# Optimization experiments

Hardware: AMD Instinct MI355X
Metric: run time of the kernel (lower is better)

The kernel has to match this reference:

```python
import jax, jax.numpy as jnp
import numpy as np

BIN_ALPHA = 1.0  # alpha mixture factor from init
NEG_SLOPE = 0.1  # LeakyReLU slope


def setup_inputs() -> dict:
    key = jax.random.key(0)
    ks = jax.random.split(key, 10)
    B, N, BIN, D = 8, 19264, 100, 768
    gene_expression = jax.random.uniform(ks[0], (B, N), dtype=jnp.float32) * 10.0
    pad_mask = jax.random.randint(ks[1], (B, N), 0, 2, dtype=jnp.int32)
    masked_mask = jax.random.randint(ks[2], (B, N), 0, 2, dtype=jnp.int32)
    # layer1: Linear(1, BIN) -> weight (BIN,1) stored as (BIN,), bias (BIN,)
    w1 = jax.random.normal(ks[3], (BIN,), dtype=jnp.float32) * (1.0)
    b1 = jax.random.normal(ks[4], (BIN,), dtype=jnp.float32) * 0.1
    # layer2: Linear(BIN, BIN) -> weight (BIN,BIN), bias (BIN,)
    w2 = jax.random.normal(ks[5], (BIN, BIN), dtype=jnp.float32) * (1.0 / np.sqrt(BIN))
    b2 = jax.random.normal(ks[6], (BIN,), dtype=jnp.float32) * 0.1
    emb_table = jax.random.normal(ks[7], (BIN, D), dtype=jnp.float32)
    pad_emb = jax.random.normal(ks[8], (D,), dtype=jnp.float32)
    mask_emb = jax.random.normal(ks[9], (D,), dtype=jnp.float32)
    return {
        "gene_expression": gene_expression,
        "pad_mask": pad_mask,
        "masked_mask": masked_mask,
        "w1": w1, "b1": b1, "w2": w2, "b2": b2,
        "emb_table": emb_table, "pad_emb": pad_emb, "mask_emb": mask_emb,
    }


def reference(gene_expression, pad_mask, masked_mask, w1, b1, w2, b2,
              emb_table, pad_emb, mask_emb):
    # v1 = Linear(1, BIN): x[..., None] * w1 + b1 -> (B, N, BIN)
    v1 = gene_expression[..., None] * w1 + b1
    # LeakyReLU(0.1)
    v2 = jnp.where(v1 > 0, v1, NEG_SLOPE * v1)
    # cross-layer projection: v3 = alpha * v2 + Linear(BIN, BIN)(v2)
    v3 = BIN_ALPHA * v2 + jnp.einsum("bnk,jk->bnj", v2, w2) + b2
    weights = jax.nn.softmax(v3, axis=-1)          # (B, N, BIN)
    embeddings = jnp.einsum("bnk,kd->bnd", weights, emb_table)  # (B, N, D)
    # mixed_precision=True: pad/mask token embeddings are cast to bfloat16
    # before being scattered into the float32 output (then upcast on assign).
    pad_e = pad_emb.astype(jnp.bfloat16).astype(embeddings.dtype)
    mask_e = mask_emb.astype(jnp.bfloat16).astype(embeddings.dtype)
    embeddings = jnp.where((pad_mask != 0)[..., None], pad_e, embeddings)
    embeddings = jnp.where((masked_mask != 0)[..., None], mask_e, embeddings)
    return embeddings
```

## Files before the change

### kernel.cpp

```cpp
#include <hip/hip_runtime.h>
#include <hip/hip_bf16.h>

#define BINS 100
#define DIM 768
#define TPB 64
#define NTHREADS 256
#define KPAD 128
#define PITCH 136

#define OFF_ET    0
#define OFF_P     196608
#define OFF_Q     197120
#define OFF_RARE  197632
#define OFF_R     199680
#define OFF_W2PT  199744

typedef __attribute__((ext_vector_type(8))) short bf16x8;
typedef __attribute__((ext_vector_type(4))) float f32x4;
typedef __attribute__((ext_vector_type(16))) float f32x16;

__device__ __forceinline__ unsigned short f2bf(float x) {
    __hip_bfloat16 h = __float2bfloat16(x);
    return *reinterpret_cast<unsigned short*>(&h);
}
__device__ __forceinline__ float bfrt(float x) {
    return __bfloat162float(__float2bfloat16(x));
}
__device__ __forceinline__ f32x4 bfrt4(f32x4 v) {
    f32x4 r;
    r.x = bfrt(v.x); r.y = bfrt(v.y); r.z = bfrt(v.z); r.w = bfrt(v.w);
    return r;
}

__global__ void prep(const float* __restrict__ emb,
                     const float* __restrict__ w1,
                     const float* __restrict__ b1,
                     const float* __restrict__ w2,
                     const float* __restrict__ b2,
                     unsigned char* __restrict__ ws)
{
    const int bid = blockIdx.x;
    const int tid = threadIdx.x;
    if (bid < DIM) {
        unsigned short* et = (unsigned short*)(ws + OFF_ET);
        float v = (tid < BINS) ? emb[(long)tid * DIM + bid] : 0.f;
        et[bid * KPAD + tid] = f2bf(v);
        return;
    }
    __shared__ float pl[BINS], ql[BINS], tl[BINS];
    float* Pv   = (float*)(ws + OFF_P);
    float* Qv   = (float*)(ws + OFF_Q);
    f32x4* rare = (f32x4*)(ws + OFF_RARE);
    int*   Rp   = (int*)  (ws + OFF_R);
    float* w2pT = (float*)(ws + OFF_W2PT);
    if (tid < BINS) {
        float w = w1[tid], b = b1[tid];
        float f = (w > 0.f || (w == 0.f && b > 0.f)) ? 1.f : 0.1f;
        pl[tid] = w * f;
        ql[tid] = b * f;
        tl[tid] = (w != 0.f) ? (-b / w) : -1.f;
    }
    __syncthreads();
    if (tid < BINS) {
        const int j = tid;
        float P = pl[j];
        float Q = ql[j] + b2[j];
        for (int k = 0; k < BINS; k++) {
            float w = w2[j * BINS + k];
            P = fmaf(w, pl[k], P);
            Q = fmaf(w, ql[k], Q);
            w2pT[k * BINS + j] = w + (j == k ? 1.f : 0.f);
        }
        Pv[j] = P; Qv[j] = Q;
        float tk = tl[tid];
        int rank = 0;
        for (int k2 = 0; k2 < BINS; k2++) {
            float t2 = tl[k2];
            rank += (t2 > tk || (t2 == tk && k2 < tid)) ? 1 : 0;
        }
        f32x4 e;
        e.x = tk; e.y = w1[tid]; e.z = b1[tid];
        e.w = __int_as_float(tid);
        rare[rank] = e;
    }
    if (tid == 0) {
        int R = 0;
        for (int k = 0; k < BINS; k++) R += (tl[k] > 0.f) ? 1 : 0;
        *Rp = R;
        f32x4 s; s.x = -1e30f; s.y = 0.f; s.z = 0.f; s.w = __int_as_float(0);
        rare[BINS] = s;
    }
}

__global__ __launch_bounds__(NTHREADS, 8)
void ead_kernel(const float* __restrict__ gene,
                const int*   __restrict__ pad_mask,
                const int*   __restrict__ masked_mask,
                const unsigned short* __restrict__ et,
                const float* __restrict__ Pv,
                const float* __restrict__ Qv,
                const f32x4* __restrict__ rare,
                const int*   __restrict__ Rp,
                const float* __restrict__ w2pT,
                const float* __restrict__ pad_emb,
                const float* __restrict__ mask_emb,
                float* __restrict__ out,
                int T)
{
    __shared__ unsigned short wbf[TPB][PITCH];
    __shared__ float xs[TPB];
    __shared__ short surv[TPB];
    __shared__ short olist[TPB];
    __shared__ int Ssh, Osh;

    const int tid  = threadIdx.x;
    const int lane = tid & 63;
    const int wave = tid >> 6;

    const int nblk = (int)gridDim.x;
    const int bid  = (int)blockIdx.x;
    const int wg   = ((nblk & 7) == 0) ? ((bid & 7) * (nblk >> 3) + (bid >> 3))
                                       : bid;
    const long t0  = (long)wg * TPB;
    const int nvalid = min(TPB, (int)(T - t0));

    if (wave == 0) {
        int o = 3;
        if (lane < nvalid) {
            int pm  = pad_mask[t0 + lane];
            int msk = masked_mask[t0 + lane];
            o = msk ? 2 : (pm ? 1 : 0);
            xs[lane] = gene[t0 + lane];
        }
        unsigned long long bs = __ballot(o == 0);
        unsigned long long bo = __ballot(o == 1 || o == 2);
        int si = __popcll(bs & ((1ull << lane) - 1ull));
        int oi = __popcll(bo & ((1ull << lane) - 1ull));
        if (o == 0) surv[si] = (short)lane;
        if (o == 1 || o == 2) olist[oi] = (short)(lane | ((o == 2) ? 256 : 0));
        if (lane == 0) { Ssh = __popcll(bs); Osh = __popcll(bo); }
    }
    __syncthreads();
    const int S = Ssh, O = Osh;

    {
        const f32x4* pe = (const f32x4*)pad_emb;
        const f32x4* me = (const f32x4*)mask_emb;
        f32x4 p0 = bfrt4(pe[lane]), p1 = bfrt4(pe[lane + 64]), p2 = bfrt4(pe[lane + 128]);
        f32x4 m0 = bfrt4(me[lane]), m1 = bfrt4(me[lane + 64]), m2 = bfrt4(me[lane + 128]);
        for (int i = wave; i < O; i += 4) {
            int e = olist[i];
            int row = e & 63;
            bool mm = (e & 256) != 0;
            f32x4* orow = (f32x4*)(out + (t0 + row) * (long)DIM);
            __builtin_nontemporal_store(mm ? m0 : p0, orow + lane);
            __builtin_nontemporal_store(mm ? m1 : p1, orow + lane + 64);
            __builtin_nontemporal_store(mm ? m2 : p2, orow + lane + 128);
        }
    }

    {
        int s = wave + 4 * (lane >> 2);
        int part = lane & 3;
        const int j0 = part * 25;
        if (s < S) {
            float x = xs[surv[s]];
            float v3[25];
            #pragma unroll
            for (int i = 0; i < 25; i++)
                v3[i] = fmaf(x, Pv[j0 + i], Qv[j0 + i]);
            const int R = *Rp;
            for (int idx = 0; idx < R; ++idx) {
                f32x4 rr = rare[idx];
                if (rr.x <= x) break;
                float v1 = fmaf(x, rr.y, rr.z);
                float d = 0.9f * fabsf(v1);
                int k = __float_as_int(rr.w);
                const float* wc = w2pT + k * BINS + j0;
                #pragma unroll
                for (int i = 0; i < 25; i++)
                    v3[i] = fmaf(wc[i], d, v3[i]);
            }
            float vmax = -1e30f;
            #pragma unroll
            for (int i = 0; i < 25; i++) vmax = fmaxf(vmax, v3[i]);
            vmax = fmaxf(vmax, __shfl_xor(vmax, 1));
            vmax = fmaxf(vmax, __shfl_xor(vmax, 2));
            float sum = 0.f;
            #pragma unroll
            for (int i = 0; i < 25; i++) {
                v3[i] = __expf(v3[i] - vmax);
                sum += v3[i];
            }
            sum += __shfl_xor(sum, 1);
            sum += __shfl_xor(sum, 2);
            float inv = 1.f / sum;
            #pragma unroll
            for (int i = 0; i < 25; i++)
                wbf[s][j0 + i] = f2bf(v3[i] * inv);
            if (part == 3) {
                #pragma unroll
                for (int j = BINS; j < KPAD; j += 2)
                    *reinterpret_cast<unsigned int*>(&wbf[s][j]) = 0u;
            }
        }
    }
    __syncthreads();

    if (S > 0) {
        const int col  = lane & 31;
        const int half = lane >> 5;
        const int nmt = (S > 32) ? 2 : 1;
        for (int mtile = 0; mtile < nmt; mtile++) {
            const unsigned short* arow = &wbf[mtile * 32 + col][half * 8];
            bf16x8 a0 = *(const bf16x8*)(arow);
            bf16x8 a1 = *(const bf16x8*)(arow + 16);
            bf16x8 a2 = *(const bf16x8*)(arow + 32);
            bf16x8 a3 = *(const bf16x8*)(arow + 48);
            bf16x8 a4 = *(const bf16x8*)(arow + 64);
            bf16x8 a5 = *(const bf16x8*)(arow + 80);
            bf16x8 a6 = *(const bf16x8*)(arow + 96);
            bf16x8 a7 = *(const bf16x8*)(arow + 112);
            for (int ct = 0; ct < 6; ct++) {
                int cbase = (wave * 6 + ct) * 32;
                const unsigned short* bp = et + (long)(cbase + col) * KPAD + half * 8;
                f32x16 acc;
                #pragma unroll
                for (int r = 0; r < 16; r++) acc[r] = 0.f;
                acc = __builtin_amdgcn_mfma_f32_32x32x16_bf16(a0, *(const bf16x8*)(bp),       acc, 0, 0, 0);
                acc = __builtin_amdgcn_mfma_f32_32x32x16_bf16(a1, *(const bf16x8*)(bp + 16),  acc, 0, 0, 0);
                acc = __builtin_amdgcn_mfma_f32_32x32x16_bf16(a2, *(const bf16x8*)(bp + 32),  acc, 0, 0, 0);
                acc = __builtin_amdgcn_mfma_f32_32x32x16_bf16(a3, *(const bf16x8*)(bp + 48),  acc, 0, 0, 0);
                acc = __builtin_amdgcn_mfma_f32_32x32x16_bf16(a4, *(const bf16x8*)(bp + 64),  acc, 0, 0, 0);
                acc = __builtin_amdgcn_mfma_f32_32x32x16_bf16(a5, *(const bf16x8*)(bp + 80),  acc, 0, 0, 0);
                acc = __builtin_amdgcn_mfma_f32_32x32x16_bf16(a6, *(const bf16x8*)(bp + 96),  acc, 0, 0, 0);
                acc = __builtin_amdgcn_mfma_f32_32x32x16_bf16(a7, *(const bf16x8*)(bp + 112), acc, 0, 0, 0);
                #pragma unroll
                for (int r = 0; r < 16; r++) {
                    int row = (r & 3) + 8 * (r >> 2) + 4 * half + mtile * 32;
                    if (row < S) {
                        int tkn = surv[row];
                        out[(t0 + tkn) * (long)DIM + cbase + col] = acc[r];
                    }
                }
            }
        }
    }
}

extern "C" void kernel_launch(void* const* d_in, const int* in_sizes, int n_in,
                              void* d_out, int out_size, void* d_ws, size_t ws_size,
                              hipStream_t stream) {
    const float* gene  = (const float*)d_in[0];
    const int*   pm    = (const int*)  d_in[1];
    const int*   mm    = (const int*)  d_in[2];
    const float* w1    = (const float*)d_in[3];
    const float* b1    = (const float*)d_in[4];
    const float* w2    = (const float*)d_in[5];
    const float* b2    = (const float*)d_in[6];
    const float* emb   = (const float*)d_in[7];
    const float* pade  = (const float*)d_in[8];
    const float* maske = (const float*)d_in[9];
    float* out = (float*)d_out;
    unsigned char* ws = (unsigned char*)d_ws;

    int T = in_sizes[0];
    int nblk = (T + TPB - 1) / TPB;

    hipLaunchKernelGGL(prep, dim3(DIM + 1), dim3(KPAD), 0, stream,
                       emb, w1, b1, w2, b2, ws);
    hipLaunchKernelGGL(ead_kernel, dim3(nblk), dim3(NTHREADS), 0, stream,
                       gene, pm, mm,
                       (const unsigned short*)(ws + OFF_ET),
                       (const float*)(ws + OFF_P),
                       (const float*)(ws + OFF_Q),
                       (const f32x4*)(ws + OFF_RARE),
                       (const int*)(ws + OFF_R),
                       (const float*)(ws + OFF_W2PT),
                       pade, maske, out, T);
}
```

Measured before the change: 146.9 us.

## Transpose MFMA tiling to 16x16x32 with embedding as A operand and row-vector stores

```diff
diff --git a/kernel.cpp b/kernel.cpp
--- a/kernel.cpp
+++ b/kernel.cpp
@@ -17,7 +17,6 @@
 
 typedef __attribute__((ext_vector_type(8))) short bf16x8;
 typedef __attribute__((ext_vector_type(4))) float f32x4;
-typedef __attribute__((ext_vector_type(16))) float f32x16;
 
 __device__ __forceinline__ unsigned short f2bf(float x) {
     __hip_bfloat16 h = __float2bfloat16(x);
@@ -142,22 +141,6 @@
     }
     __syncthreads();
     const int S = Ssh, O = Osh;
-
-    {
-        const f32x4* pe = (const f32x4*)pad_emb;
-        const f32x4* me = (const f32x4*)mask_emb;
-        f32x4 p0 = bfrt4(pe[lane]), p1 = bfrt4(pe[lane + 64]), p2 = bfrt4(pe[lane + 128]);
-        f32x4 m0 = bfrt4(me[lane]), m1 = bfrt4(me[lane + 64]), m2 = bfrt4(me[lane + 128]);
-        for (int i = wave; i < O; i += 4) {
-            int e = olist[i];
-            int row = e & 63;
-            bool mm = (e & 256) != 0;
-            f32x4* orow = (f32x4*)(out + (t0 + row) * (long)DIM);
-            __builtin_nontemporal_store(mm ? m0 : p0, orow + lane);
-            __builtin_nontemporal_store(mm ? m1 : p1, orow + lane + 64);
-            __builtin_nontemporal_store(mm ? m2 : p2, orow + lane + 128);
-        }
-    }
 
     {
         int s = wave + 4 * (lane >> 2);
@@ -207,45 +190,92 @@
     }
     __syncthreads();
 
-    if (S > 0) {
-        const int col  = lane & 31;
-        const int half = lane >> 5;
-        const int nmt = (S > 32) ? 2 : 1;
-        for (int mtile = 0; mtile < nmt; mtile++) {
-            const unsigned short* arow = &wbf[mtile * 32 + col][half * 8];
-            bf16x8 a0 = *(const bf16x8*)(arow);
-            bf16x8 a1 = *(const bf16x8*)(arow + 16);
-            bf16x8 a2 = *(const bf16x8*)(arow + 32);
-            bf16x8 a3 = *(const bf16x8*)(arow + 48);
-            bf16x8 a4 = *(const bf16x8*)(arow + 64);
-            bf16x8 a5 = *(const bf16x8*)(arow + 80);
-            bf16x8 a6 = *(const bf16x8*)(arow + 96);
-            bf16x8 a7 = *(const bf16x8*)(arow + 112);
-            for (int ct = 0; ct < 6; ct++) {
-                int cbase = (wave * 6 + ct) * 32;
-                const unsigned short* bp = et + (long)(cbase + col) * KPAD + half * 8;
-                f32x16 acc;
-                #pragma unroll
-                for (int r = 0; r < 16; r++) acc[r] = 0.f;
-                acc = __builtin_amdgcn_mfma_f32_32x32x16_bf16(a0, *(const bf16x8*)(bp),       acc, 0, 0, 0);
-                acc = __builtin_amdgcn_mfma_f32_32x32x16_bf16(a1, *(const bf16x8*)(bp + 16),  acc, 0, 0, 0);
-                acc = __builtin_amdgcn_mfma_f32_32x32x16_bf16(a2, *(const bf16x8*)(bp + 32),  acc, 0, 0, 0);
-                acc = __builtin_amdgcn_mfma_f32_32x32x16_bf16(a3, *(const bf16x8*)(bp + 48),  acc, 0, 0, 0);
-                acc = __builtin_amdgcn_mfma_f32_32x32x16_bf16(a4, *(const bf16x8*)(bp + 64),  acc, 0, 0, 0);
-                acc = __builtin_amdgcn_mfma_f32_32x32x16_bf16(a5, *(const bf16x8*)(bp + 80),  acc, 0, 0, 0);
-                acc = __builtin_amdgcn_mfma_f32_32x32x16_bf16(a6, *(const bf16x8*)(bp + 96),  acc, 0, 0, 0);
-                acc = __builtin_amdgcn_mfma_f32_32x32x16_bf16(a7, *(const bf16x8*)(bp + 112), acc, 0, 0, 0);
-                #pragma unroll
-                for (int r = 0; r < 16; r++) {
-                    int row = (r & 3) + 8 * (r >> 2) + 4 * half + mtile * 32;
-                    if (row < S) {
-                        int tkn = surv[row];
-                        out[(t0 + tkn) * (long)DIM + cbase + col] = acc[r];
-                    }
-                }
-            }
-        }
-    }
+    const int arow  = lane & 15;
+    const int kgrp  = lane >> 4;
+    const int dbase = wave * 192;
+    const f32x4* pe = (const f32x4*)pad_emb;
+    const f32x4* me = (const f32x4*)mask_emb;
+    f32x4 pv0 = pe[lane], pv1 = pe[lane + 64], pv2 = pe[lane + 128];
+    f32x4 mv0 = me[lane], mv1 = me[lane + 64], mv2 = me[lane + 128];
+    bf16x8 afrA[4], afrB[4];
+    {
+        const unsigned short* ap0 = et + (long)(dbase + arow) * KPAD + kgrp * 8;
+        const unsigned short* ap1 = et + (long)(dbase + 16 + arow) * KPAD + kgrp * 8;
+        #pragma unroll
+        for (int kss = 0; kss < 4; kss++) afrA[kss] = *(const bf16x8*)(ap0 + kss * 32);
+        #pragma unroll
+        for (int kss = 0; kss < 4; kss++) afrB[kss] = *(const bf16x8*)(ap1 + kss * 32);
+    }
+
+    {
+        f32x4 p0 = bfrt4(pv0), p1 = bfrt4(pv1), p2 = bfrt4(pv2);
+        f32x4 m0 = bfrt4(mv0), m1 = bfrt4(mv1), m2 = bfrt4(mv2);
+        for (int i = wave; i < O; i += 4) {
+            int e = olist[i];
+            int row = e & 63;
+            bool mm = (e & 256) != 0;
+            f32x4* orow = (f32x4*)(out + (t0 + row) * (long)DIM);
+            __builtin_nontemporal_store(mm ? m0 : p0, orow + lane);
+            __builtin_nontemporal_store(mm ? m1 : p1, orow + lane + 64);
+            __builtin_nontemporal_store(mm ? m2 : p2, orow + lane + 128);
+        }
+    }
+
+    const int SM = (S + 15) >> 4;
+    int tok0, tok1, tok2, tok3;
+    {
+        int sl;
+        sl = 0 * 16 + arow; tok0 = (sl < S) ? surv[sl] : -1;
+        sl = 1 * 16 + arow; tok1 = (SM > 1 && sl < S) ? surv[sl] : -1;
+        sl = 2 * 16 + arow; tok2 = (SM > 2 && sl < S) ? surv[sl] : -1;
+        sl = 3 * 16 + arow; tok3 = (SM > 3 && sl < S) ? surv[sl] : -1;
+    }
+
+#define CBODY(cc, CUR)                                                          \
+    do {                                                                        \
+        f32x4 acc[4];                                                           \
+        _Pragma("unroll")                                                       \
+        for (int mt = 0; mt < 4; mt++) {                                        \
+            if (mt < SM) {                                                      \
+                f32x4 a = {0.f, 0.f, 0.f, 0.f};                                 \
+                _Pragma("unroll")                                               \
+                for (int kss = 0; kss < 4; kss++) {                             \
+                    bf16x8 bfr = *(const bf16x8*)&wbf[mt * 16 + arow]           \
+                                                    [kss * 32 + kgrp * 8];      \
+                    a = __builtin_amdgcn_mfma_f32_16x16x32_bf16(CUR[kss], bfr,  \
+                                                                a, 0, 0, 0);    \
+                }                                                               \
+                acc[mt] = a;                                                    \
+            }                                                                   \
+        }                                                                       \
+        if ((cc) < 10) {   \
+            const unsigned short* apn =                                         \
+                et + (long)(dbase + ((cc) + 2) * 16 + arow) * KPAD + kgrp * 8;  \
+            _Pragma("unroll")                                                   \
+            for (int kss = 0; kss < 4; kss++)                                   \
+                CUR[kss] = *(const bf16x8*)(apn + kss * 32);                    \
+        }                                                                       \
+        {                                                                       \
+            int dt = dbase + (cc) * 16;                                         \
+            if (tok0 >= 0)                                                      \
+                *(f32x4*)(out + (t0 + tok0) * (long)DIM + dt + kgrp * 4) = acc[0]; \
+            if (SM > 1 && tok1 >= 0)                                            \
+                *(f32x4*)(out + (t0 + tok1) * (long)DIM + dt + kgrp * 4) = acc[1]; \
+            if (SM > 2 && tok2 >= 0)                                            \
+                *(f32x4*)(out + (t0 + tok2) * (long)DIM + dt + kgrp * 4) = acc[2]; \
+            if (SM > 3 && tok3 >= 0)                                            \
+                *(f32x4*)(out + (t0 + tok3) * (long)DIM + dt + kgrp * 4) = acc[3]; \
+        }                                                                       \
+    } while (0)
+
+    if (SM > 0) {
+        #pragma unroll
+        for (int cc = 0; cc < 6; cc++) {
+            CBODY(2 * cc, afrA);
+            CBODY(2 * cc + 1, afrB);
+        }
+    }
+#undef CBODY
 }
 
 extern "C" void kernel_launch(void* const* d_in, const int* in_sizes, int n_in,
```

After: 163.4 us. 1.11x slower.
